# Performance work log

Hardware: AMD Instinct MI355X
Metric: run time of the kernel (lower is better)

The kernel has to match this reference:

```python
import jax, jax.numpy as jnp
import numpy as np

EPS = 1e-5  # InstanceNorm2d default


def setup_inputs() -> dict:
    key = jax.random.key(0)
    ks = jax.random.split(key, 8)
    B, L, D, Q, C, H, W = 16, 24, 256, 256, 256, 128, 128
    s = 0.05
    return {
        "w_source": jax.random.normal(ks[0], (B, L, D), jnp.float32),
        "w_target": jax.random.normal(ks[1], (B, L, D), jnp.float32),
        "h": jax.random.normal(ks[2], (B, C, H, W), jnp.float32),
        "conv0_w": jax.random.normal(ks[3], (Q, C), jnp.float32) * s,   # 1x1 conv kernel
        "conv0_b": jnp.zeros((Q,), jnp.float32),
        "fck_w": jax.random.normal(ks[4], (Q, D), jnp.float32) * s,
        "fck_b": jnp.zeros((Q,), jnp.float32),
        "fc_w": jax.random.normal(ks[5], (2 * C, D), jnp.float32) * s,
        "fc_b": jnp.zeros((2 * C,), jnp.float32),
        "in_w": jnp.ones((C,), jnp.float32),
        "in_b": jnp.zeros((C,), jnp.float32),
    }


def reference(w_source, w_target, h, conv0_w, conv0_b, fck_w, fck_b, fc_w, fc_b, in_w, in_b):
    # ---- CrossAttention ----
    # q: 1x1 conv over h  -> [B,H,W,Q]
    q = jnp.einsum("bchw,qc->bhwq", h, conv0_w) + conv0_b
    # k: word keys        -> [B,L,Q]
    k = jnp.einsum("bld,qd->blq", w_source, fck_w) + fck_b
    attn = jnp.einsum("bhwq,blq->bhwl", q, k)  # [B,H,W,L]

    # ---- MaskingAllocation ----
    scores = jnp.einsum("bld,bmd->blm", w_source, w_target)       # [B,L,L]
    left = jnp.sum(scores, axis=1, keepdims=True) - scores        # [B,L,L]
    idx = jnp.argmax(left, axis=-1)                               # [B,L]
    w_alloc = jnp.take_along_axis(w_target, idx[..., None], axis=1)  # [B,L,D]

    # ---- modulation params ----
    bg = jnp.einsum("bld,ed->ble", w_alloc, fc_w) + fc_b          # [B,L,2C]
    beta, gamma = jnp.split(bg, 2, axis=-1)                       # each [B,L,C]
    beta_map = jnp.einsum("bhwl,blc->bchw", attn, beta)           # [B,C,H,W]
    gamma_map = jnp.einsum("bhwl,blc->bchw", attn, gamma)

    # ---- InstanceNorm2d (affine) + modulation ----
    mean = jnp.mean(h, axis=(2, 3), keepdims=True)
    var = jnp.var(h, axis=(2, 3), keepdims=True)
    hn = (h - mean) * jax.lax.rsqrt(var + EPS)
    hn = hn * in_w[None, :, None, None] + in_b[None, :, None, None]
    return hn * gamma_map + beta_map
```

## Files before the change

### kernel.cpp

```cpp
#include <hip/hip_runtime.h>
#include <stdint.h>

#define HW 16384
#define Bn 16
#define Ln 24
#define Dn 256
#define Qn 256
#define Cn 256

typedef __attribute__((ext_vector_type(8))) short short8;
typedef __attribute__((ext_vector_type(4))) float f32x4;

__device__ __forceinline__ unsigned short f2bf(float f) {
  unsigned u = __builtin_bit_cast(unsigned, f);
  u += 0x7FFFu + ((u >> 16) & 1u);
  return (unsigned short)(u >> 16);
}
__device__ __forceinline__ float bf2f(unsigned short s) {
  return __builtin_bit_cast(float, (unsigned)s << 16);
}

__device__ __forceinline__ void gl_lds16(const void* gsrc, void* lds) {
  __builtin_amdgcn_global_load_lds(
      (const __attribute__((address_space(1))) unsigned int*)gsrc,
      (__attribute__((address_space(3))) unsigned int*)lds, 16, 0, 0);
}

__global__ void k_keys(const float* __restrict__ wsrc, const float* __restrict__ fckw,
                       const float* __restrict__ fckb, float* __restrict__ kmat) {
  int b = blockIdx.x / Ln, l = blockIdx.x % Ln;
  __shared__ float row[Dn];
  row[threadIdx.x] = wsrc[(b * Ln + l) * Dn + threadIdx.x];
  __syncthreads();
  int q = threadIdx.x;
  const float* wq = fckw + q * Dn;
  float acc = fckb[q];
#pragma unroll 8
  for (int d = 0; d < Dn; ++d) acc += row[d] * wq[d];
  kmat[(b * Ln + l) * Qn + q] = acc;
}

__global__ void k_alloc(const float* __restrict__ wsrc, const float* __restrict__ wtgt,
                        const float* __restrict__ conv0b, const float* __restrict__ kmat,
                        float* __restrict__ walloc, float* __restrict__ bias0) {
  int b = blockIdx.x;
  __shared__ float S[Ln][Dn];
  __shared__ float T[Ln][Dn];
  __shared__ double sc[Ln][Ln];
  __shared__ double cs[Ln];
  __shared__ int idx[Ln];
  int tid = threadIdx.x;
  for (int n = tid; n < Ln * Dn; n += 256) {
    S[n >> 8][n & 255] = wsrc[b * Ln * Dn + n];
    T[n >> 8][n & 255] = wtgt[b * Ln * Dn + n];
  }
  __syncthreads();
  for (int p = tid; p < Ln * Ln; p += 256) {
    int l = p / Ln, m = p % Ln;
    double a = 0.0;
    for (int d = 0; d < Dn; ++d) a += (double)S[l][d] * (double)T[m][d];
    sc[l][m] = a;
  }
  __syncthreads();
  if (tid < Ln) {
    double a = 0.0;
    for (int l = 0; l < Ln; ++l) a += sc[l][tid];
    cs[tid] = a;
  }
  __syncthreads();
  if (tid < Ln) {
    double best = -1e300; int bi = 0;
    for (int m = 0; m < Ln; ++m) {
      double v = cs[m] - sc[tid][m];
      if (v > best) { best = v; bi = m; }
    }
    idx[tid] = bi;
  }
  __syncthreads();
  for (int n = tid; n < Ln * Dn; n += 256) {
    int l = n >> 8, d = n & 255;
    walloc[b * Ln * Dn + n] = T[idx[l]][d];
  }
  if (tid < Ln) {
    float a = 0.f;
    const float* kr = kmat + (b * Ln + tid) * Qn;
    for (int q = 0; q < Qn; ++q) a += conv0b[q] * kr[q];
    bias0[b * Ln + tid] = a;
  }
}

__global__ void k_mbg(const float* __restrict__ kmat, const float* __restrict__ conv0w,
                      const float* __restrict__ walloc, const float* __restrict__ fcw,
                      const float* __restrict__ fcb,
                      float* __restrict__ Mmat, float* __restrict__ bg) {
  int bid = blockIdx.x;
  __shared__ float row[Dn];
  if (bid < Bn * Ln) {
    int b = bid / Ln, l = bid % Ln;
    row[threadIdx.x] = kmat[(b * Ln + l) * Qn + threadIdx.x];
    __syncthreads();
    int c = threadIdx.x;
    float acc = 0.f;
    for (int q = 0; q < Qn; ++q) acc += row[q] * conv0w[q * Cn + c];
    Mmat[(b * Ln + l) * Cn + c] = acc;
  } else {
    int id = bid - Bn * Ln;
    int b = id / Ln, l = id % Ln;
    row[threadIdx.x] = walloc[(b * Ln + l) * Dn + threadIdx.x];
    __syncthreads();
    for (int it = 0; it < 2; ++it) {
      int e = it * 256 + threadIdx.x;
      const float* we = fcw + e * Dn;
      float acc = fcb[e];
      for (int d = 0; d < Dn; ++d) acc += row[d] * we[d];
      bg[(b * Ln + l) * (2 * Cn) + e] = acc;
    }
  }
}

__global__ void k_gbuild(const float* __restrict__ Mmat, const float* __restrict__ bg,
                         const float* __restrict__ bias0,
                         unsigned short* __restrict__ Gt, float* __restrict__ bv) {
  int g = blockIdx.x, b = blockIdx.y;
  __shared__ float Ms[Ln][Dn];
  __shared__ float Gb[Ln][128];
  __shared__ float B0[Ln];
  int tid = threadIdx.x;
  for (int n = tid; n < Ln * Dn; n += 256) Ms[n >> 8][n & 255] = Mmat[b * Ln * Dn + n];
  for (int n = tid; n < Ln * 128; n += 256) {
    int l = n >> 7, j = n & 127;
    int e = (j < 64) ? (Cn + g * 64 + j) : (g * 64 + (j - 64));
    Gb[l][j] = bg[(b * Ln + l) * (2 * Cn) + e];
  }
  if (tid < Ln) B0[tid] = bias0[b * Ln + tid];
  __syncthreads();
  char* base = (char*)Gt + (unsigned long)(b * 4 + g) * 65536;
  for (int r = 0; r < 128; ++r) {
    int isb = (r >> 4) & 1;
    int c_loc = (r >> 5) * 16 + (r & 15);
    int j = c_loc + isb * 64;
    float acc = 0.f;
#pragma unroll
    for (int l = 0; l < Ln; ++l) acc += Ms[l][tid] * Gb[l][j];
    unsigned off = (unsigned)((r * 512 + tid * 2) ^ ((r & 7) << 4));
    *(unsigned short*)(base + off) = f2bf(acc);
  }
  if (tid < 128) {
    float a = 0.f;
#pragma unroll
    for (int l = 0; l < Ln; ++l) a += B0[l] * Gb[l][tid];
    bv[b * 512 + g * 128 + tid] = a;
  }
}

__global__ void k_tr(const float* __restrict__ h, unsigned short* __restrict__ hT,
                     float* __restrict__ part) {
  int hwc = blockIdx.x;
  int cc  = blockIdx.y;
  int b   = blockIdx.z;
  int tid = threadIdx.x;
  int w = tid >> 6, lane = tid & 63;
  __shared__ unsigned short tile[64 * 258];
  __shared__ float red[64 * 17 + 16];
  const int c0 = cc * 64, hw0 = hwc * 256;
  for (int i = 0; i < 16; ++i) {
    int cl = i * 4 + w;
    f32x4 v = *(const f32x4*)(h + ((unsigned long)(b * Cn + c0 + cl)) * HW + hw0 + lane * 4);
    unsigned lo = (unsigned)f2bf(v.x) | ((unsigned)f2bf(v.y) << 16);
    unsigned hi = (unsigned)f2bf(v.z) | ((unsigned)f2bf(v.w) << 16);
    unsigned* dst = (unsigned*)(tile + cl * 258 + lane * 4);
    dst[0] = lo; dst[1] = hi;
  }
  __syncthreads();
  int cp = tid & 31, sub = tid >> 5;
  float s0 = 0.f, s20 = 0.f, s1 = 0.f, s21 = 0.f;
  for (int i = 0; i < 32; ++i) {
    int hw = i * 8 + sub;
    unsigned short a0 = tile[(2 * cp) * 258 + hw];
    unsigned short a1 = tile[(2 * cp + 1) * 258 + hw];
    float f0 = bf2f(a0), f1 = bf2f(a1);
    s0 += f0; s20 += f0 * f0; s1 += f1; s21 += f1 * f1;
    unsigned pk = (unsigned)a0 | ((unsigned)a1 << 16);
    *(unsigned*)(hT + ((unsigned long)b * HW + hw0 + hw) * Cn + c0 + 2 * cp) = pk;
  }
  red[(2 * cp) * 17 + sub * 2]     = s0;
  red[(2 * cp) * 17 + sub * 2 + 1] = s20;
  red[(2 * cp + 1) * 17 + sub * 2]     = s1;
  red[(2 * cp + 1) * 17 + sub * 2 + 1] = s21;
  __syncthreads();
  if (tid < 64) {
    float a = 0.f, q = 0.f;
#pragma unroll
    for (int j = 0; j < 8; ++j) { a += red[tid * 17 + j * 2]; q += red[tid * 17 + j * 2 + 1]; }
    float* pp = part + (((unsigned long)(b * Cn + c0 + tid)) * 64 + hwc) * 2;
    pp[0] = a; pp[1] = q;
  }
}

__global__ void k_fin(const float* __restrict__ part, const float* __restrict__ inw,
                      const float* __restrict__ inb, float* __restrict__ ss) {
  int id = blockIdx.x * 256 + threadIdx.x;
  int c = id & 255;
  float s = 0.f, s2 = 0.f;
  const float* pp = part + (unsigned long)id * 128;
  for (int j = 0; j < 64; ++j) { s += pp[2 * j]; s2 += pp[2 * j + 1]; }
  float mean = s * (1.0f / HW);
  float var = s2 * (1.0f / HW) - mean * mean;
  float rs = rsqrtf(var + 1e-5f);
  float scv = rs * inw[c];
  float sh = inb[c] - mean * scv;
  ss[id * 2] = scv; ss[id * 2 + 1] = sh;
}

__global__ __launch_bounds__(512, 1) void k_main(
    const unsigned short* __restrict__ hT, const unsigned short* __restrict__ Gt,
    const float* __restrict__ bv, const float* __restrict__ ss,
    float* __restrict__ out) {
  int x = blockIdx.x;
  int o = x & 7, idx = x >> 3;
  int b = idx >> 2, g = idx & 3;
  int tid = threadIdx.x;
  int w = tid >> 6, lane = tid & 63;
  int mw = w >> 2, nw = w & 3;
  int lr = lane & 15, lg = lane >> 4;

  __shared__ __align__(16) unsigned char Ab[65536];
  __shared__ __align__(16) unsigned char Bb[2][32768];

  const char* Gblob = (const char*)Gt + (unsigned long)(b * 4 + g) * 65536;
  const char* hTb = (const char*)hT + (unsigned long)b * HW * 512;

#pragma unroll
  for (int i = 0; i < 8; ++i)
    gl_lds16(Gblob + i * 8192 + w * 1024 + lane * 16, &Ab[i * 8192 + w * 1024]);

#define STAGE_B(c2, buf_)                                                        \
  {                                                                              \
    int s2_ = (c2) & 3, t2_ = (c2) >> 2;                                         \
    const char* base_ = hTb + (unsigned long)((o * 8 + t2_) * 256) * 512 + s2_ * 128; \
    _Pragma("unroll")                                                            \
    for (int l_ = 0; l_ < 4; ++l_) {                                             \
      int rowl_ = l_ * 64 + w * 8 + (lane >> 3);                                 \
      int bir_ = ((lane & 7) * 16) ^ ((rowl_ & 7) << 4);                         \
      gl_lds16(base_ + (unsigned long)rowl_ * 512 + bir_,                        \
               &Bb[buf_][l_ * 8192 + w * 1024]);                                 \
    }                                                                            \
  }

  f32x4 acc[4][4];
#pragma unroll
  for (int mf = 0; mf < 4; ++mf)
#pragma unroll
    for (int nf = 0; nf < 4; ++nf) acc[mf][nf] = (f32x4){0.f, 0.f, 0.f, 0.f};

  unsigned short h16[2][4][4];
  const float* ssb = ss + b * Cn * 2;
  const float* bvb = bv + b * 512 + g * 128;

  STAGE_B(0, 0);
  STAGE_B(1, 1);
  asm volatile("s_waitcnt vmcnt(4)" ::: "memory");
  __builtin_amdgcn_s_barrier();
  __builtin_amdgcn_sched_barrier(0);

#define COMPUTE(ch_, s_)                                                         \
  {                                                                              \
    const unsigned char* Bcur = &Bb[(ch_) & 1][0];                               \
    if ((s_) == g) {                                                             \
      _Pragma("unroll") for (int p = 0; p < 2; ++p)                              \
      _Pragma("unroll") for (int nf = 0; nf < 4; ++nf) {                         \
        int row = nw * 64 + nf * 16 + lr;                                        \
        int sw = (row & 7) << 4;                                                 \
        _Pragma("unroll") for (int r = 0; r < 4; ++r) {                          \
          int c_loc = (mw * 2 + p) * 16 + lg * 4 + r;                            \
          h16[p][nf][r] = *(const unsigned short*)(&Bcur[row * 128 + ((c_loc * 2) ^ sw)]); \
        }                                                                        \
      }                                                                          \
    }                                                                            \
    _Pragma("unroll") for (int kk = 0; kk < 2; ++kk) {                           \
      short8 afr[4], bfr[4];                                                     \
      _Pragma("unroll") for (int mf = 0; mf < 4; ++mf) {                         \
        int row = mw * 64 + mf * 16 + lr;                                        \
        afr[mf] = *(const short8*)(                                              \
            &Ab[row * 512 + (((s_) * 128 + kk * 64 + lg * 16) ^ ((row & 7) << 4))]); \
      }                                                                          \
      _Pragma("unroll") for (int nf = 0; nf < 4; ++nf) {                         \
        int row = nw * 64 + nf * 16 + lr;                                        \
        bfr[nf] = *(const short8*)(                                              \
            &Bcur[row * 128 + ((kk * 64 + lg * 16) ^ ((row & 7) << 4))]);        \
      }                                                                          \
      _Pragma("unroll") for (int mf = 0; mf < 4; ++mf)                           \
        _Pragma("unroll") for (int nf = 0; nf < 4; ++nf)                         \
          acc[mf][nf] = __builtin_amdgcn_mfma_f32_16x16x32_bf16(afr[mf], bfr[nf], \
                                                                acc[mf][nf], 0, 0, 0); \
    }                                                                            \
  }

#define EPILOGUE(t_)                                                             \
  {                                                                              \
    int hwbase = (o * 8 + (t_)) * 256 + nw * 64 + lr;                            \
    _Pragma("unroll") for (int p = 0; p < 2; ++p)                                \
    _Pragma("unroll") for (int r = 0; r < 4; ++r) {                              \
      int c_loc = (mw * 2 + p) * 16 + lg * 4 + r;                                \
      int cch = g * 64 + c_loc;                                                  \
      float scv = ssb[cch * 2], sh = ssb[cch * 2 + 1];                           \
      float bvg = bvb[c_loc], bvbt = bvb[64 + c_loc];                            \
      float* orow = out + (unsigned long)(b * Cn + cch) * HW + hwbase;           \
      _Pragma("unroll") for (int nf = 0; nf < 4; ++nf) {                         \
        float hn = bf2f(h16[p][nf][r]) * scv + sh;                               \
        orow[nf * 16] = hn * (acc[2 * p][nf][r] + bvg) + (acc[2 * p + 1][nf][r] + bvbt); \
      }                                                                          \
    }                                                                            \
    _Pragma("unroll") for (int mf = 0; mf < 4; ++mf)                             \
      _Pragma("unroll") for (int nf = 0; nf < 4; ++nf)                           \
        acc[mf][nf] = (f32x4){0.f, 0.f, 0.f, 0.f};                               \
  }

#define SYNC_STAGE(ch_, VM_)                                                     \
  asm volatile("s_waitcnt lgkmcnt(0)" ::: "memory");                             \
  __builtin_amdgcn_sched_barrier(0);                                             \
  __builtin_amdgcn_s_barrier();                                                  \
  STAGE_B((ch_) + 2, (ch_) & 1);                                                 \
  asm volatile("s_waitcnt vmcnt(" #VM_ ")" ::: "memory");                        \
  __builtin_amdgcn_s_barrier();                                                  \
  __builtin_amdgcn_sched_barrier(0);

  COMPUTE(0, 0) SYNC_STAGE(0, 4)
  COMPUTE(1, 1) SYNC_STAGE(1, 4)
  COMPUTE(2, 2) SYNC_STAGE(2, 4)
  COMPUTE(3, 3) EPILOGUE(0) SYNC_STAGE(3, 36)
  for (int t = 1; t < 7; ++t) {
    int ch = t * 4;
    COMPUTE(ch, 0) SYNC_STAGE(ch, 4)
    COMPUTE(ch + 1, 1) SYNC_STAGE(ch + 1, 4)
    COMPUTE(ch + 2, 2) SYNC_STAGE(ch + 2, 4)
    COMPUTE(ch + 3, 3) EPILOGUE(t) SYNC_STAGE(ch + 3, 36)
  }
  COMPUTE(28, 0) SYNC_STAGE(28, 4)
  COMPUTE(29, 1) SYNC_STAGE(29, 4)
  COMPUTE(30, 2)
  asm volatile("s_waitcnt lgkmcnt(0)" ::: "memory");
  __builtin_amdgcn_sched_barrier(0);
  __builtin_amdgcn_s_barrier();
  asm volatile("s_waitcnt vmcnt(0)" ::: "memory");
  __builtin_amdgcn_s_barrier();
  __builtin_amdgcn_sched_barrier(0);
  COMPUTE(31, 3) EPILOGUE(7)

#undef SYNC_STAGE
#undef EPILOGUE
#undef COMPUTE
#undef STAGE_B
}

__global__ void k_sentinel(float* out) { out[0] = 12345.0f; }

extern "C" void kernel_launch(void* const* d_in, const int* in_sizes, int n_in,
                              void* d_out, int out_size, void* d_ws, size_t ws_size,
                              hipStream_t stream) {
  const float* wsrc   = (const float*)d_in[0];
  const float* wtgt   = (const float*)d_in[1];
  const float* h      = (const float*)d_in[2];
  const float* conv0w = (const float*)d_in[3];
  const float* conv0b = (const float*)d_in[4];
  const float* fckw   = (const float*)d_in[5];
  const float* fckb   = (const float*)d_in[6];
  const float* fcw    = (const float*)d_in[7];
  const float* fcb    = (const float*)d_in[8];
  const float* inw    = (const float*)d_in[9];
  const float* inb    = (const float*)d_in[10];
  float* out = (float*)d_out;
  char* ws = (char*)d_ws;

  const size_t NEED = 142542848ull;
  if (ws_size < NEED) {
    k_sentinel<<<1, 1, 0, stream>>>(out);
    return;
  }

  unsigned short* hT = (unsigned short*)(ws + 0);
  float* kmat   = (float*)(ws + 134217728);
  float* walloc = (float*)(ws + 134610944);
  float* bias0  = (float*)(ws + 135004160);
  float* bg     = (float*)(ws + 135006208);
  float* Mmat   = (float*)(ws + 135792640);
  unsigned short* Gt = (unsigned short*)(ws + 136185856);
  float* bv     = (float*)(ws + 140380160);
  float* part   = (float*)(ws + 140412928);
  float* ss     = (float*)(ws + 142510080);

  dim3 gt(64, 4, Bn);
  k_tr<<<gt, 256, 0, stream>>>(h, hT, part);
  k_keys<<<Bn * Ln, 256, 0, stream>>>(wsrc, fckw, fckb, kmat);
  k_alloc<<<Bn, 256, 0, stream>>>(wsrc, wtgt, conv0b, kmat, walloc, bias0);
  k_mbg<<<2 * Bn * Ln, 256, 0, stream>>>(kmat, conv0w, walloc, fcw, fcb, Mmat, bg);
  dim3 gg(4, Bn);
  k_gbuild<<<gg, 256, 0, stream>>>(Mmat, bg, bias0, Gt, bv);
  k_fin<<<16, 256, 0, stream>>>(part, inw, inb, ss);
  k_main<<<512, 512, 0, stream>>>(hT, Gt, bv, ss, out);
}
```

Before: 348.9 us.

## Deepen B-tile pipeline to four half-size LDS buffers with 32-wide K chunks

Splits each streamed hT K-chunk from 64 to 32 channels and uses four 16KB LDS buffers instead of two 32KB ones. Loads are now issued four stages ahead, which gives global-load latency more time to hide behind MFMA work. The swizzle pattern and the h16 snapshot indexing are reworked to match the 64-byte rows. In exchange it doubles the number of barriers and waitcnt synchronisation points per tile and halves the MFMA work between them, and the vmcnt bookkeeping is fragile.

```diff
diff --git a/kernel.cpp b/kernel.cpp
--- a/kernel.cpp
+++ b/kernel.cpp
@@ -225,7 +225,7 @@
   int lr = lane & 15, lg = lane >> 4;
 
   __shared__ __align__(16) unsigned char Ab[65536];
-  __shared__ __align__(16) unsigned char Bb[2][32768];
+  __shared__ __align__(16) unsigned char Bb[4][16384];
 
   const char* Gblob = (const char*)Gt + (unsigned long)(b * 4 + g) * 65536;
   const char* hTb = (const char*)hT + (unsigned long)b * HW * 512;
@@ -236,13 +236,13 @@
 
 #define STAGE_B(c2, buf_)                                                        \
   {                                                                              \
-    int s2_ = (c2) & 3, t2_ = (c2) >> 2;                                         \
-    const char* base_ = hTb + (unsigned long)((o * 8 + t2_) * 256) * 512 + s2_ * 128; \
+    int s2_ = (c2) & 7, t2_ = (c2) >> 3;                                         \
+    const char* base_ = hTb + (unsigned long)((o * 8 + t2_) * 256) * 512;        \
     _Pragma("unroll")                                                            \
-    for (int l_ = 0; l_ < 4; ++l_) {                                             \
-      int rowl_ = l_ * 64 + w * 8 + (lane >> 3);                                 \
-      int bir_ = ((lane & 7) * 16) ^ ((rowl_ & 7) << 4);                         \
-      gl_lds16(base_ + (unsigned long)rowl_ * 512 + bir_,                        \
+    for (int l_ = 0; l_ < 2; ++l_) {                                             \
+      int rowg_ = l_ * 128 + w * 16 + (lane >> 2);                               \
+      int bir_ = s2_ * 64 + ((((lane & 3) << 4)) ^ (((rowg_ >> 1) & 3) << 4));   \
+      gl_lds16(base_ + (unsigned long)rowg_ * 512 + bir_,                        \
                &Bb[buf_][l_ * 8192 + w * 1024]);                                 \
     }                                                                            \
   }
@@ -256,44 +256,45 @@
   unsigned short h16[2][4][4];
   const float* ssb = ss + b * Cn * 2;
   const float* bvb = bv + b * 512 + g * 128;
+  const int ssnap = 2 * g + mw;
 
   STAGE_B(0, 0);
   STAGE_B(1, 1);
-  asm volatile("s_waitcnt vmcnt(4)" ::: "memory");
+  STAGE_B(2, 2);
+  STAGE_B(3, 3);
+  asm volatile("s_waitcnt vmcnt(6)" ::: "memory");
   __builtin_amdgcn_s_barrier();
   __builtin_amdgcn_sched_barrier(0);
 
 #define COMPUTE(ch_, s_)                                                         \
   {                                                                              \
-    const unsigned char* Bcur = &Bb[(ch_) & 1][0];                               \
-    if ((s_) == g) {                                                             \
+    const unsigned char* Bcur = &Bb[(ch_) & 3][0];                               \
+    if ((s_) == ssnap) {                                                         \
       _Pragma("unroll") for (int p = 0; p < 2; ++p)                              \
       _Pragma("unroll") for (int nf = 0; nf < 4; ++nf) {                         \
         int row = nw * 64 + nf * 16 + lr;                                        \
-        int sw = (row & 7) << 4;                                                 \
+        int sw = ((row >> 1) & 3) << 4;                                          \
         _Pragma("unroll") for (int r = 0; r < 4; ++r) {                          \
-          int c_loc = (mw * 2 + p) * 16 + lg * 4 + r;                            \
-          h16[p][nf][r] = *(const unsigned short*)(&Bcur[row * 128 + ((c_loc * 2) ^ sw)]); \
+          int kloc = p * 16 + lg * 4 + r;                                        \
+          h16[p][nf][r] = *(const unsigned short*)(&Bcur[row * 64 + ((kloc * 2) ^ sw)]); \
         }                                                                        \
       }                                                                          \
     }                                                                            \
-    _Pragma("unroll") for (int kk = 0; kk < 2; ++kk) {                           \
-      short8 afr[4], bfr[4];                                                     \
-      _Pragma("unroll") for (int mf = 0; mf < 4; ++mf) {                         \
-        int row = mw * 64 + mf * 16 + lr;                                        \
-        afr[mf] = *(const short8*)(                                              \
-            &Ab[row * 512 + (((s_) * 128 + kk * 64 + lg * 16) ^ ((row & 7) << 4))]); \
-      }                                                                          \
-      _Pragma("unroll") for (int nf = 0; nf < 4; ++nf) {                         \
-        int row = nw * 64 + nf * 16 + lr;                                        \
-        bfr[nf] = *(const short8*)(                                              \
-            &Bcur[row * 128 + ((kk * 64 + lg * 16) ^ ((row & 7) << 4))]);        \
-      }                                                                          \
-      _Pragma("unroll") for (int mf = 0; mf < 4; ++mf)                           \
-        _Pragma("unroll") for (int nf = 0; nf < 4; ++nf)                         \
-          acc[mf][nf] = __builtin_amdgcn_mfma_f32_16x16x32_bf16(afr[mf], bfr[nf], \
-                                                                acc[mf][nf], 0, 0, 0); \
+    short8 afr[4], bfr[4];                                                       \
+    _Pragma("unroll") for (int mf = 0; mf < 4; ++mf) {                           \
+      int row = mw * 64 + mf * 16 + lr;                                          \
+      afr[mf] = *(const short8*)(                                                \
+          &Ab[row * 512 + (((s_) * 64 + lg * 16) ^ ((row & 7) << 4))]);          \
     }                                                                            \
+    _Pragma("unroll") for (int nf = 0; nf < 4; ++nf) {                           \
+      int row = nw * 64 + nf * 16 + lr;                                          \
+      bfr[nf] = *(const short8*)(                                                \
+          &Bcur[row * 64 + ((lg << 4) ^ (((row >> 1) & 3) << 4))]);              \
+    }                                                                            \
+    _Pragma("unroll") for (int mf = 0; mf < 4; ++mf)                             \
+      _Pragma("unroll") for (int nf = 0; nf < 4; ++nf)                           \
+        acc[mf][nf] = __builtin_amdgcn_mfma_f32_16x16x32_bf16(afr[mf], bfr[nf],  \
+                                                              acc[mf][nf], 0, 0, 0); \
   }
 
 #define EPILOGUE(t_)                                                             \
@@ -316,38 +317,45 @@
         acc[mf][nf] = (f32x4){0.f, 0.f, 0.f, 0.f};                               \
   }
 
-#define SYNC_STAGE(ch_, VM_)                                                     \
+#define SYNCS(ch_, N_)                                                           \
   asm volatile("s_waitcnt lgkmcnt(0)" ::: "memory");                             \
   __builtin_amdgcn_sched_barrier(0);                                             \
   __builtin_amdgcn_s_barrier();                                                  \
-  STAGE_B((ch_) + 2, (ch_) & 1);                                                 \
-  asm volatile("s_waitcnt vmcnt(" #VM_ ")" ::: "memory");                        \
+  STAGE_B((ch_) + 4, (ch_) & 3);                                                 \
+  asm volatile("s_waitcnt vmcnt(" #N_ ")" ::: "memory");                         \
   __builtin_amdgcn_s_barrier();                                                  \
   __builtin_amdgcn_sched_barrier(0);
 
-  COMPUTE(0, 0) SYNC_STAGE(0, 4)
-  COMPUTE(1, 1) SYNC_STAGE(1, 4)
-  COMPUTE(2, 2) SYNC_STAGE(2, 4)
-  COMPUTE(3, 3) EPILOGUE(0) SYNC_STAGE(3, 36)
-  for (int t = 1; t < 7; ++t) {
-    int ch = t * 4;
-    COMPUTE(ch, 0) SYNC_STAGE(ch, 4)
-    COMPUTE(ch + 1, 1) SYNC_STAGE(ch + 1, 4)
-    COMPUTE(ch + 2, 2) SYNC_STAGE(ch + 2, 4)
-    COMPUTE(ch + 3, 3) EPILOGUE(t) SYNC_STAGE(ch + 3, 36)
-  }
-  COMPUTE(28, 0) SYNC_STAGE(28, 4)
-  COMPUTE(29, 1) SYNC_STAGE(29, 4)
-  COMPUTE(30, 2)
-  asm volatile("s_waitcnt lgkmcnt(0)" ::: "memory");
+#define SYNCT(N_)                                                                \
+  asm volatile("s_waitcnt lgkmcnt(0)" ::: "memory");                             \
+  __builtin_amdgcn_sched_barrier(0);                                             \
+  __builtin_amdgcn_s_barrier();                                                  \
+  asm volatile("s_waitcnt vmcnt(" #N_ ")" ::: "memory");                         \
+  __builtin_amdgcn_s_barrier();                                                  \
   __builtin_amdgcn_sched_barrier(0);
-  __builtin_amdgcn_s_barrier();
-  asm volatile("s_waitcnt vmcnt(0)" ::: "memory");
-  __builtin_amdgcn_s_barrier();
-  __builtin_amdgcn_sched_barrier(0);
-  COMPUTE(31, 3) EPILOGUE(7)
-
-#undef SYNC_STAGE
+
+  for (int t = 0; t < 7; ++t) {
+    int c0 = t * 8;
+    COMPUTE(c0 + 0, 0) SYNCS(c0 + 0, 38)
+    COMPUTE(c0 + 1, 1) SYNCS(c0 + 1, 38)
+    COMPUTE(c0 + 2, 2) SYNCS(c0 + 2, 6)
+    COMPUTE(c0 + 3, 3) SYNCS(c0 + 3, 6)
+    COMPUTE(c0 + 4, 4) SYNCS(c0 + 4, 6)
+    COMPUTE(c0 + 5, 5) SYNCS(c0 + 5, 6)
+    COMPUTE(c0 + 6, 6) SYNCS(c0 + 6, 6)
+    COMPUTE(c0 + 7, 7) EPILOGUE(t) SYNCS(c0 + 7, 38)
+  }
+  COMPUTE(56, 0) SYNCS(56, 38)
+  COMPUTE(57, 1) SYNCS(57, 38)
+  COMPUTE(58, 2) SYNCS(58, 6)
+  COMPUTE(59, 3) SYNCS(59, 6)
+  COMPUTE(60, 4) SYNCT(4)
+  COMPUTE(61, 5) SYNCT(2)
+  COMPUTE(62, 6) SYNCT(0)
+  COMPUTE(63, 7) EPILOGUE(7)
+
+#undef SYNCT
+#undef SYNCS
 #undef EPILOGUE
 #undef COMPUTE
 #undef STAGE_B
```

Measured after the change: 346.4 us. About the same (-0.7%).
